# Performance work log

Measured on AMD Instinct MI355X. Metric: run time of the kernel, lower is better.

## Reference

```python
import jax, jax.numpy as jnp
import numpy as np

IH, IW = 32, 32
HEADS, DIM_HEAD = 8, 32
B, INP, OUP = 16, 384, 384
N = IH * IW
SCALE = DIM_HEAD ** -0.5


def _make_relative_index(ih, iw):
    coords = np.stack(np.meshgrid(np.arange(ih), np.arange(iw), indexing='ij'))  # [2, ih, iw]
    cf = coords.reshape(2, -1)                                                   # [2, n]
    rel = cf[:, :, None] - cf[:, None, :]                                        # [2, n, n]
    rel = rel.transpose(1, 2, 0).astype(np.int32)                                # [n, n, 2]
    rel[:, :, 0] += ih - 1
    rel[:, :, 1] += iw - 1
    rel[:, :, 0] *= 2 * iw - 1
    return rel.sum(-1)                                                           # [n, n]


def setup_inputs() -> dict:
    key = jax.random.key(0)
    k1, k2, k3, k4, k5 = jax.random.split(key, 5)
    inner = HEADS * DIM_HEAD
    x = jax.random.normal(k1, (B, N, INP), dtype=jnp.float32)
    w_qkv = jax.random.normal(k2, (INP, 3 * inner), dtype=jnp.float32) * (INP ** -0.5)
    relative_bias_table = jax.random.normal(k3, ((2 * IH - 1) * (2 * IW - 1), HEADS), dtype=jnp.float32) * 0.02
    w_out = jax.random.normal(k4, (inner, OUP), dtype=jnp.float32) * (inner ** -0.5)
    b_out = jax.random.normal(k5, (OUP,), dtype=jnp.float32) * 0.02
    relative_index = jnp.asarray(_make_relative_index(IH, IW))
    return {"x": x, "w_qkv": w_qkv, "relative_bias_table": relative_bias_table,
            "w_out": w_out, "b_out": b_out, "relative_index": relative_index}


def reference(x, w_qkv, relative_bias_table, w_out, b_out, relative_index):
    b, n, _ = x.shape
    qkv = x @ w_qkv                                              # [b, n, 3*h*d]
    q, k, v = jnp.split(qkv, 3, axis=-1)
    def heads(t):
        return t.reshape(b, n, HEADS, DIM_HEAD).transpose(0, 2, 1, 3)  # [b, h, n, d]
    q, k, v = heads(q), heads(k), heads(v)
    dots = jnp.einsum('bhnd,bhmd->bhnm', q, k) * SCALE           # [b, h, n, n]
    bias = relative_bias_table[relative_index]                   # [n, n, h]
    dots = dots + bias.transpose(2, 0, 1)[None]                  # add [1, h, n, n]
    attn = jax.nn.softmax(dots, axis=-1)
    out = jnp.einsum('bhnm,bhmd->bhnd', attn, v)                 # [b, h, n, d]
    out = out.transpose(0, 2, 1, 3).reshape(b, n, HEADS * DIM_HEAD)
    return out @ w_out + b_out
```

## Files before the change

kernel.cpp:

```cpp
#include <hip/hip_runtime.h>
#include <hip/hip_fp16.h>

typedef unsigned short u16;
typedef __attribute__((ext_vector_type(4))) short s16x4;
typedef __attribute__((ext_vector_type(8))) short s16x8;
typedef __attribute__((ext_vector_type(4))) _Float16 h16x4;
typedef __attribute__((ext_vector_type(4))) float f32x4;

#define SCALE_Q 0.17677669529663687f

static __device__ __forceinline__ u16 f2h16(float v) {
    __half h = __float2half(v);
    return __builtin_bit_cast(u16, h);
}
static __device__ __forceinline__ void async16(const void* g, void* l) {
    __builtin_amdgcn_global_load_lds(
        (const __attribute__((address_space(1))) void*)g,
        (__attribute__((address_space(3))) void*)l, 16, 0, 0);
}
static __device__ __forceinline__ f32x4 mfmaH(h16x4 a, h16x4 b, f32x4 c) {
    return __builtin_amdgcn_mfma_f32_16x16x16f16(a, b, c, 0, 0, 0);
}

__global__ __launch_bounds__(256) void prep_kernel(
    const float* __restrict__ x, const float* __restrict__ wqkv,
    const float* __restrict__ wout,
    u16* __restrict__ Xh, u16* __restrict__ Wq, u16* __restrict__ Wo)
{
    int bid = blockIdx.x, tid = threadIdx.x;
    if (bid < 1536) {
        int t = bid * 256 + tid;
#pragma unroll
        for (int i = 0; i < 4; ++i) {
            int idx = t + i * 393216;
            float4 v = ((const float4*)x)[idx];
            ushort4 o;
            o.x = f2h16(v.x); o.y = f2h16(v.y); o.z = f2h16(v.z); o.w = f2h16(v.w);
            ((ushort4*)Xh)[idx] = o;
        }
    } else if (bid < 2688) {
        int t = (bid - 1536) * 256 + tid;
        int n = t / 384, k = t - n * 384;
        Wq[t] = f2h16(wqkv[(size_t)k * 768 + n]);
    } else {
        int t = (bid - 2688) * 256 + tid;
        int n = t / 256, k = t - n * 256;
        Wo[t] = f2h16(wout[(size_t)k * 384 + n]);
    }
}

template<int KSEG, int BN, int NTOT, int MODE>
__global__ __launch_bounds__(256) void gemm_h(
    const u16* __restrict__ A, const u16* __restrict__ Bt,
    u16* __restrict__ Qb, u16* __restrict__ Kb, u16* __restrict__ Vb,
    const float* __restrict__ bias, float* __restrict__ Cout)
{
    constexpr int KT = KSEG / 64;
    constexpr int nct = NTOT / BN;
    constexpr int nwg = 128 * nct;
    constexpr int cpx = nwg / 8;
    constexpr int bjN = BN / 32;
    constexpr int BCH = BN * 8 / 256;
    int u = (blockIdx.x % 8) * cpx + blockIdx.x / 8;
    int rt = u / nct, ct = u - rt * nct;
    int r0 = rt * 128, c0 = ct * BN;

    __shared__ u16 At[2][128 * 64];
    __shared__ u16 Bts[2][BN * 64];

    int tid = threadIdx.x;
    int w = tid >> 6, lane = tid & 63, g = lane >> 4, c15 = lane & 15;
    int r0w = (w >> 1) * 64, c0w = (w & 1) * (BN / 2);

    f32x4 acc[4][bjN];
    const f32x4 z4 = {0.f, 0.f, 0.f, 0.f};
#pragma unroll
    for (int a = 0; a < 4; ++a)
#pragma unroll
        for (int b = 0; b < bjN; ++b) acc[a][b] = z4;

    auto stage = [&](int buf, int kt) {
        int k0 = kt * 64;
#pragma unroll
        for (int it = 0; it < 4; ++it) {
            int chunk = (it * 4 + w) * 64 + lane;
            int rr = chunk >> 3;
            int uu = (chunk & 7) ^ (rr & 7);
            async16(A + (size_t)(r0 + rr) * KSEG + k0 + uu * 8,
                    &At[buf][(it * 4 + w) * 512]);
        }
#pragma unroll
        for (int it = 0; it < BCH; ++it) {
            int chunk = (it * 4 + w) * 64 + lane;
            int rr = chunk >> 3;
            int uu = (chunk & 7) ^ (rr & 7);
            async16(Bt + (size_t)(c0 + rr) * KSEG + k0 + uu * 8,
                    &Bts[buf][(it * 4 + w) * 512]);
        }
    };

    stage(0, 0);
    __syncthreads();
    int cur = 0;
    for (int kt = 0; kt < KT; ++kt) {
        if (kt + 1 < KT) stage(cur ^ 1, kt + 1);
#pragma unroll
        for (int ks = 0; ks < 4; ++ks) {
            h16x4 af[4], bfr[bjN];
            int bc = (ks * 16 + 4 * g) * 2;
#pragma unroll
            for (int ai = 0; ai < 4; ++ai) {
                int row = r0w + 16 * ai + c15;
                int off = row * 128 + (bc ^ ((row & 7) << 4));
                af[ai] = *(const h16x4*)((const char*)At[cur] + off);
            }
#pragma unroll
            for (int bj = 0; bj < bjN; ++bj) {
                int row = c0w + 16 * bj + c15;
                int off = row * 128 + (bc ^ ((row & 7) << 4));
                bfr[bj] = *(const h16x4*)((const char*)Bts[cur] + off);
            }
#pragma unroll
            for (int ai = 0; ai < 4; ++ai)
#pragma unroll
                for (int bj = 0; bj < bjN; ++bj)
                    acc[ai][bj] = mfmaH(af[ai], bfr[bj], acc[ai][bj]);
        }
        __syncthreads();
        cur ^= 1;
    }

#pragma unroll
    for (int ai = 0; ai < 4; ++ai)
#pragma unroll
        for (int bj = 0; bj < bjN; ++bj)
#pragma unroll
            for (int i = 0; i < 4; ++i) {
                int R = r0 + r0w + 16 * ai + 4 * g + i;
                int c = c0 + c0w + 16 * bj + c15;
                float v = acc[ai][bj][i];
                if (MODE == 0) {
                    int bb = R >> 10, n = R & 1023;
                    int which = c >> 8, hd = c & 255;
                    int hh = hd >> 5, d = hd & 31;
                    size_t o = ((size_t)(bb * 8 + hh) * 1024 + n) * 32 + d;
                    if (which == 0)      Qb[o] = f2h16(v * SCALE_Q);
                    else if (which == 1) Kb[o] = f2h16(v);
                    else                 Vb[o] = f2h16(v);
                } else {
                    Cout[(size_t)R * NTOT + c] = v + bias[c];
                }
            }
}

__global__ __launch_bounds__(256) void transpose_v_kernel(
    const u16* __restrict__ Vb, u16* __restrict__ Vtg)
{
    int bid = blockIdx.x;
    int mc = bid & 7, bh = bid >> 3;
    int m0 = mc * 128;
    __shared__ u16 t[128 * 36];
    const u16* src = Vb + (size_t)bh * 32768 + (size_t)m0 * 32;
    int tid = threadIdx.x;
#pragma unroll
    for (int it = 0; it < 4; ++it) {
        int c = it * 256 + tid;
        int m = c >> 3, d0 = (c & 7) * 4;
        s16x4 v = *(const s16x4*)(src + c * 4);
        *(s16x4*)(&t[m * 36 + d0]) = v;
    }
    __syncthreads();
    u16* dst = Vtg + (size_t)bh * 32768 + m0;
#pragma unroll
    for (int j = 0; j < 16; ++j) {
        int o = j * 256 + tid;
        int d = o >> 7, m = o & 127;
        dst[(size_t)d * 1024 + m] = t[m * 36 + d];
    }
}

__global__ __launch_bounds__(256) void attn_kernel(
    const u16* __restrict__ Qb, const u16* __restrict__ Kb, const u16* __restrict__ Vtg,
    const float* __restrict__ table, u16* __restrict__ Oh)
{
    int u = (blockIdx.x % 8) * 128 + blockIdx.x / 8;
    int qt = u & 7, h = (u >> 3) & 7, b = u >> 6;
    int bh = b * 8 + h;
    int tid = threadIdx.x;
    int w = tid >> 6, lane = tid & 63, g = lane >> 4, c15 = lane & 15;

    __shared__ float tbl[2205];
    __shared__ u16 KtL[2][64 * 40];
    __shared__ u16 VtL[2][32 * 72];

    int rowbase = 4 * qt * 63;
    for (int i = tid; i < 2205; i += 256) tbl[i] = table[(size_t)(rowbase + i) * 8 + h];

    h16x4 qf[2][2];
    int cbase[2];
#pragma unroll
    for (int qs = 0; qs < 2; ++qs) {
        int nq = qt * 128 + w * 32 + qs * 16 + c15;
        const u16* qp = Qb + ((size_t)bh * 1024 + nq) * 32 + 4 * g;
        qf[qs][0] = *(const h16x4*)qp;
        qf[qs][1] = *(const h16x4*)(qp + 16);
        int yn = nq >> 5, xn = nq & 31;
        cbase[qs] = (yn - 4 * qt + 31) * 63 + (xn + 31);
    }

    float lsum[2] = {0.f, 0.f};
    f32x4 Oa[2][2];
    const f32x4 z4 = {0.f, 0.f, 0.f, 0.f};
#pragma unroll
    for (int qs = 0; qs < 2; ++qs) { Oa[qs][0] = z4; Oa[qs][1] = z4; }

    const u16* kgb = Kb + (size_t)bh * 32768;
    const u16* vgb = Vtg + (size_t)bh * 32768;

    {
        int r = tid >> 2, uu = tid & 3;
        s16x8 kv = *(const s16x8*)(kgb + (size_t)r * 32 + uu * 8);
        *(s16x8*)(&KtL[0][r * 40 + uu * 8]) = kv;
        int r2 = tid >> 3, u2 = tid & 7;
        s16x8 vv = *(const s16x8*)(vgb + (size_t)r2 * 1024 + u2 * 8);
        *(s16x8*)(&VtL[0][r2 * 72 + u2 * 8]) = vv;
    }
    __syncthreads();

    int p = 0;
    for (int mt = 0; mt < 16; ++mt) {
        s16x8 kNext, vNext;
        bool more = (mt < 15);
        if (more) {
            int m0 = (mt + 1) * 64;
            kNext = *(const s16x8*)(kgb + (size_t)(m0 + (tid >> 2)) * 32 + (tid & 3) * 8);
            vNext = *(const s16x8*)(vgb + (size_t)(tid >> 3) * 1024 + m0 + (tid & 7) * 8);
        }
#pragma unroll
        for (int qs = 0; qs < 2; ++qs) {
#pragma unroll
            for (int ms = 0; ms < 4; ++ms) {
                const u16* kr = &KtL[p][(ms * 16 + c15) * 40 + 4 * g];
                h16x4 kf0 = *(const h16x4*)kr;
                h16x4 kf1 = *(const h16x4*)(kr + 16);
                f32x4 st = z4;
                st = mfmaH(kf0, qf[qs][0], st);
                st = mfmaH(kf1, qf[qs][1], st);
                int mbase = mt * 64 + ms * 16 + 4 * g;
                int idxb = cbase[qs] - mbase - 31 * (mbase >> 5);
                h16x4 pfm;
                float ls = 0.f;
#pragma unroll
                for (int i = 0; i < 4; ++i) {
                    float pv = __expf(st[i] + tbl[idxb - i]);
                    ls += pv;
                    pfm[i] = (_Float16)pv;
                }
                lsum[qs] += ls;
                const u16* vr = &VtL[p][c15 * 72 + ms * 16 + 4 * g];
                h16x4 vf0 = *(const h16x4*)vr;
                h16x4 vf1 = *(const h16x4*)(vr + 16 * 72);
                Oa[qs][0] = mfmaH(pfm, vf0, Oa[qs][0]);
                Oa[qs][1] = mfmaH(pfm, vf1, Oa[qs][1]);
            }
        }
        if (more) {
            *(s16x8*)(&KtL[p ^ 1][(tid >> 2) * 40 + (tid & 3) * 8]) = kNext;
            *(s16x8*)(&VtL[p ^ 1][(tid >> 3) * 72 + (tid & 7) * 8]) = vNext;
        }
        __syncthreads();
        p ^= 1;
    }

#pragma unroll
    for (int qs = 0; qs < 2; ++qs) {
        float l = lsum[qs];
        l += __shfl_xor(l, 16);
        l += __shfl_xor(l, 32);
        float linv = 1.f / l;
        f32x4 lv;
#pragma unroll
        for (int i = 0; i < 4; ++i) lv[i] = __shfl(linv, 4 * g + i);
#pragma unroll
        for (int half = 0; half < 2; ++half)
#pragma unroll
            for (int i = 0; i < 4; ++i) {
                float v = Oa[qs][half][i] * lv[i];
                int n = qt * 128 + w * 32 + qs * 16 + 4 * g + i;
                size_t row = (size_t)b * 1024 + n;
                int col = h * 32 + half * 16 + c15;
                Oh[row * 256 + col] = f2h16(v);
            }
    }
}

extern "C" void kernel_launch(void* const* d_in, const int* in_sizes, int n_in,
                              void* d_out, int out_size, void* d_ws, size_t ws_size,
                              hipStream_t stream) {
    const float* x     = (const float*)d_in[0];
    const float* wqkv  = (const float*)d_in[1];
    const float* table = (const float*)d_in[2];
    const float* wout  = (const float*)d_in[3];
    const float* bout  = (const float*)d_in[4];
    float* out = (float*)d_out;

    char* ws = (char*)d_ws;
    size_t off = 0;
    auto alloc = [&](size_t bytes) -> char* {
        char* p = ws + off;
        off += (bytes + 255) & ~(size_t)255;
        return p;
    };
    u16* Xh  = (u16*)alloc(16384ull * 384 * 2);
    u16* WqT = (u16*)alloc(768ull * 384 * 2);
    u16* WoT = (u16*)alloc(384ull * 256 * 2);
    u16* Qb  = (u16*)alloc(128ull * 1024 * 32 * 2);
    u16* Kb  = (u16*)alloc(128ull * 1024 * 32 * 2);
    u16* Vb  = (u16*)alloc(128ull * 1024 * 32 * 2);
    u16* Vtg = (u16*)alloc(128ull * 1024 * 32 * 2);
    u16* Oh  = (u16*)alloc(16384ull * 256 * 2);

    prep_kernel<<<dim3(3072), dim3(256), 0, stream>>>(x, wqkv, wout, Xh, WqT, WoT);

    gemm_h<384, 192, 768, 0><<<dim3(512), dim3(256), 0, stream>>>(
        Xh, WqT, Qb, Kb, Vb, nullptr, nullptr);

    transpose_v_kernel<<<dim3(1024), dim3(256), 0, stream>>>(Vb, Vtg);

    attn_kernel<<<dim3(1024), dim3(256), 0, stream>>>(Qb, Kb, Vtg, table, Oh);

    gemm_h<256, 64, 384, 1><<<dim3(768), dim3(256), 0, stream>>>(
        Oh, WoT, nullptr, nullptr, nullptr, bout, out);
}
```

Measured before the change: 166.7 us.

## Switch attention to 16x16x32 MFMA with permuted K/V layouts and exp2 softmax

Replaces pairs of 16x16x16 f16 MFMAs in the attention inner loop with single 16x16x32 MFMAs. Q, K and transposed V are written in a permuted dim/key order so each lane loads contiguous 8-wide fragments. Softmax now uses exp2, with log2e folded into the Q scale and the bias table. The table is duplicated with a parity offset to allow paired 8-byte loads, probabilities are packed with cvt_pkrtz, and row sums are accumulated with fdot2. Launch bounds now request 4 blocks per CU, and the larger table buffer raises shared memory use, which may constrain occupancy.

```diff
diff --git a/kernel.cpp b/kernel.cpp
--- a/kernel.cpp
+++ b/kernel.cpp
@@ -2,12 +2,18 @@
 #include <hip/hip_fp16.h>
 
 typedef unsigned short u16;
+typedef unsigned int u32;
 typedef __attribute__((ext_vector_type(4))) short s16x4;
 typedef __attribute__((ext_vector_type(8))) short s16x8;
 typedef __attribute__((ext_vector_type(4))) _Float16 h16x4;
+typedef __attribute__((ext_vector_type(8))) _Float16 h16x8;
+typedef __attribute__((ext_vector_type(2))) _Float16 h16x2;
 typedef __attribute__((ext_vector_type(4))) float f32x4;
+typedef __attribute__((ext_vector_type(2))) float f32x2;
+typedef __attribute__((ext_vector_type(4))) u32 u32x4;
 
 #define SCALE_Q 0.17677669529663687f
+#define LOG2E   1.44269504088896f
 
 static __device__ __forceinline__ u16 f2h16(float v) {
     __half h = __float2half(v);
@@ -20,6 +26,22 @@
 }
 static __device__ __forceinline__ f32x4 mfmaH(h16x4 a, h16x4 b, f32x4 c) {
     return __builtin_amdgcn_mfma_f32_16x16x16f16(a, b, c, 0, 0, 0);
+}
+static __device__ __forceinline__ f32x4 mfma32(h16x8 a, h16x8 b, f32x4 c) {
+    return __builtin_amdgcn_mfma_f32_16x16x32_f16(a, b, c, 0, 0, 0);
+}
+static __device__ __forceinline__ float fexp2(float x) {
+#if __has_builtin(__builtin_amdgcn_exp2f)
+    return __builtin_amdgcn_exp2f(x);
+#else
+    return __expf(0.6931471805599453f * x);
+#endif
+}
+static __device__ __forceinline__ h16x2 cvt_pk(float a, float b) {
+    return __builtin_bit_cast(h16x2, __builtin_amdgcn_cvt_pkrtz(a, b));
+}
+static __device__ __forceinline__ int perm32(int v) {
+    return (v & ~31) | (((v >> 2) & 3) << 3) | (((v >> 4) & 1) << 2) | (v & 3);
 }
 
 __global__ __launch_bounds__(256) void prep_kernel(
@@ -143,10 +165,10 @@
                     int bb = R >> 10, n = R & 1023;
                     int which = c >> 8, hd = c & 255;
                     int hh = hd >> 5, d = hd & 31;
-                    size_t o = ((size_t)(bb * 8 + hh) * 1024 + n) * 32 + d;
-                    if (which == 0)      Qb[o] = f2h16(v * SCALE_Q);
-                    else if (which == 1) Kb[o] = f2h16(v);
-                    else                 Vb[o] = f2h16(v);
+                    size_t rowb = ((size_t)(bb * 8 + hh) * 1024 + n) * 32;
+                    if (which == 0)      Qb[rowb + perm32(d)] = f2h16(v * (SCALE_Q * LOG2E));
+                    else if (which == 1) Kb[rowb + perm32(d)] = f2h16(v);
+                    else                 Vb[rowb + d] = f2h16(v);
                 } else {
                     Cout[(size_t)R * NTOT + c] = v + bias[c];
                 }
@@ -175,11 +197,11 @@
     for (int j = 0; j < 16; ++j) {
         int o = j * 256 + tid;
         int d = o >> 7, m = o & 127;
-        dst[(size_t)d * 1024 + m] = t[m * 36 + d];
-    }
-}
-
-__global__ __launch_bounds__(256) void attn_kernel(
+        dst[(size_t)d * 1024 + perm32(m)] = t[m * 36 + d];
+    }
+}
+
+__global__ __launch_bounds__(256, 4) void attn_kernel(
     const u16* __restrict__ Qb, const u16* __restrict__ Kb, const u16* __restrict__ Vtg,
     const float* __restrict__ table, u16* __restrict__ Oh)
 {
@@ -189,23 +211,26 @@
     int tid = threadIdx.x;
     int w = tid >> 6, lane = tid & 63, g = lane >> 4, c15 = lane & 15;
 
-    __shared__ float tbl[2205];
+    __shared__ float tblR[4416];
     __shared__ u16 KtL[2][64 * 40];
     __shared__ u16 VtL[2][32 * 72];
 
     int rowbase = 4 * qt * 63;
-    for (int i = tid; i < 2205; i += 256) tbl[i] = table[(size_t)(rowbase + i) * 8 + h];
-
-    h16x4 qf[2][2];
-    int cbase[2];
+    for (int i = tid; i < 4412; i += 256) {
+        if (i < 2205)
+            tblR[i] = table[(size_t)(rowbase + i) * 8 + h] * LOG2E;
+        else if (i >= 2208)
+            tblR[i] = table[(size_t)(rowbase + i - 2207) * 8 + h] * LOG2E;
+    }
+
+    h16x8 qf8[2];
+    int base3[2];
 #pragma unroll
     for (int qs = 0; qs < 2; ++qs) {
         int nq = qt * 128 + w * 32 + qs * 16 + c15;
-        const u16* qp = Qb + ((size_t)bh * 1024 + nq) * 32 + 4 * g;
-        qf[qs][0] = *(const h16x4*)qp;
-        qf[qs][1] = *(const h16x4*)(qp + 16);
+        qf8[qs] = *(const h16x8*)(Qb + ((size_t)bh * 1024 + nq) * 32 + 8 * g);
         int yn = nq >> 5, xn = nq & 31;
-        cbase[qs] = (yn - 4 * qt + 31) * 63 + (xn + 31);
+        base3[qs] = (yn - 4 * qt + 31) * 63 + (xn + 31) - 4 * g - 3;
     }
 
     float lsum[2] = {0.f, 0.f};
@@ -226,6 +251,10 @@
         *(s16x8*)(&VtL[0][r2 * 72 + u2 * 8]) = vv;
     }
     __syncthreads();
+
+#if __has_builtin(__builtin_amdgcn_fdot2)
+    const h16x2 kOnes = {(_Float16)1.f, (_Float16)1.f};
+#endif
 
     int p = 0;
     for (int mt = 0; mt < 16; ++mt) {
@@ -236,32 +265,50 @@
             kNext = *(const s16x8*)(kgb + (size_t)(m0 + (tid >> 2)) * 32 + (tid & 3) * 8);
             vNext = *(const s16x8*)(vgb + (size_t)(tid >> 3) * 1024 + m0 + (tid & 7) * 8);
         }
+        h16x8 kf8[4], vf8[2][2];
+#pragma unroll
+        for (int ms = 0; ms < 4; ++ms)
+            kf8[ms] = *(const h16x8*)&KtL[p][(ms * 16 + c15) * 40 + 8 * g];
+#pragma unroll
+        for (int t = 0; t < 2; ++t)
+#pragma unroll
+            for (int hf = 0; hf < 2; ++hf)
+                vf8[t][hf] = *(const h16x8*)&VtL[p][(c15 + 16 * hf) * 72 + 32 * t + 8 * g];
+
+        int Amt = -126 * mt;
 #pragma unroll
         for (int qs = 0; qs < 2; ++qs) {
+            h16x2 pk[4][2];
+            const int msoff[4] = {0, 16, 63, 79};
 #pragma unroll
             for (int ms = 0; ms < 4; ++ms) {
-                const u16* kr = &KtL[p][(ms * 16 + c15) * 40 + 4 * g];
-                h16x4 kf0 = *(const h16x4*)kr;
-                h16x4 kf1 = *(const h16x4*)(kr + 16);
-                f32x4 st = z4;
-                st = mfmaH(kf0, qf[qs][0], st);
-                st = mfmaH(kf1, qf[qs][1], st);
-                int mbase = mt * 64 + ms * 16 + 4 * g;
-                int idxb = cbase[qs] - mbase - 31 * (mbase >> 5);
-                h16x4 pfm;
-                float ls = 0.f;
-#pragma unroll
-                for (int i = 0; i < 4; ++i) {
-                    float pv = __expf(st[i] + tbl[idxb - i]);
-                    ls += pv;
-                    pfm[i] = (_Float16)pv;
-                }
-                lsum[qs] += ls;
-                const u16* vr = &VtL[p][c15 * 72 + ms * 16 + 4 * g];
-                h16x4 vf0 = *(const h16x4*)vr;
-                h16x4 vf1 = *(const h16x4*)(vr + 16 * 72);
-                Oa[qs][0] = mfmaH(pfm, vf0, Oa[qs][0]);
-                Oa[qs][1] = mfmaH(pfm, vf1, Oa[qs][1]);
+                f32x4 st = mfma32(kf8[ms], qf8[qs], z4);
+                int A = base3[qs] + Amt - msoff[ms];
+                int idx = A + (A & 1) * 2207;
+                f32x2 lo = *(const f32x2*)&tblR[idx];
+                f32x2 hi = *(const f32x2*)&tblR[idx + 2];
+                float p0 = fexp2(st[0] + hi[1]);
+                float p1 = fexp2(st[1] + hi[0]);
+                float p2 = fexp2(st[2] + lo[1]);
+                float p3 = fexp2(st[3] + lo[0]);
+                pk[ms][0] = cvt_pk(p0, p1);
+                pk[ms][1] = cvt_pk(p2, p3);
+#if __has_builtin(__builtin_amdgcn_fdot2)
+                lsum[qs] = __builtin_amdgcn_fdot2(pk[ms][0], kOnes,
+                           __builtin_amdgcn_fdot2(pk[ms][1], kOnes, lsum[qs], false), false);
+#else
+                lsum[qs] += (p0 + p1) + (p2 + p3);
+#endif
+            }
+#pragma unroll
+            for (int t = 0; t < 2; ++t) {
+                u32x4 pa_u = { __builtin_bit_cast(u32, pk[2 * t][0]),
+                               __builtin_bit_cast(u32, pk[2 * t][1]),
+                               __builtin_bit_cast(u32, pk[2 * t + 1][0]),
+                               __builtin_bit_cast(u32, pk[2 * t + 1][1]) };
+                h16x8 pa = __builtin_bit_cast(h16x8, pa_u);
+                Oa[qs][0] = mfma32(pa, vf8[t][0], Oa[qs][0]);
+                Oa[qs][1] = mfma32(pa, vf8[t][1], Oa[qs][1]);
             }
         }
         if (more) {
```

New measurement: 159.9 us. 4.1% less time.
